# Optimization experiments

Measured on AMD Instinct MI355X. Metric: run time of the kernel, lower is better.

## Reference

```python
import jax, jax.numpy as jnp
import numpy as np
from jax import lax

OC, IC, K = 256, 256, 3
PAD, STRIDE = 1, 1
NNZ = 59000
N, H, W = 32, 56, 56


def setup_inputs() -> dict:
    key = jax.random.key(0)
    k1, k2, k3, k4 = jax.random.split(key, 4)
    x = jax.random.normal(k1, (N, IC, H, W), dtype=jnp.float32)
    W_val = jax.random.normal(k2, (NNZ,), dtype=jnp.float32)
    W_idx = jax.random.randint(k3, (NNZ,), 0, OC * IC * K * K, dtype=jnp.int64)
    bias = jax.random.normal(k4, (OC,), dtype=jnp.float32)
    return {"x": x, "W_val": W_val, "W_idx": W_idx, "bias": bias}


def reference(x, W_val, W_idx, bias):
    # Scatter COO values into the dense [OC, IC, K, K] weight (duplicates sum).
    dense_w = jnp.zeros((OC * IC * K * K,), dtype=W_val.dtype).at[W_idx].add(W_val)
    dense_w = dense_w.reshape(OC, IC, K, K)
    # conv2d, NCHW / OIHW layout, stride=STRIDE, symmetric padding=PAD
    out = lax.conv_general_dilated(
        x, dense_w,
        window_strides=(STRIDE, STRIDE),
        padding=[(PAD, PAD), (PAD, PAD)],
        dimension_numbers=("NCHW", "OIHW", "NCHW"),
    )
    out = out + bias[None, :, None, None]
    return out
```

## Files before the change

kernel.cpp:

```cpp
#include <hip/hip_runtime.h>

typedef unsigned short ushort;
typedef __attribute__((ext_vector_type(8))) short bf16x8;
typedef __attribute__((ext_vector_type(4))) float f32x4;
typedef __attribute__((ext_vector_type(4))) ushort us4;

#define NBATCH 32
#define ICN 256
#define OCN 256
#define HSZ 56
#define WSZ 56
#define HP 58
#define SPAT (HP*HP)
#define KTOT 2304
#define MTOT (NBATCH*HSZ*WSZ)
#define NT   (KTOT/64)

#define XP_BYTES ((size_t)NBATCH*SPAT*ICN*2)
#define WD_BYTES ((size_t)OCN*KTOT*4)

__device__ __forceinline__ ushort f2bf(float f) {
  union { float f; unsigned u; } c; c.f = f;
  unsigned r = c.u + 0x7FFFu + ((c.u >> 16) & 1u);
  return (ushort)(r >> 16);
}

__global__ void k_transpose(const float* __restrict__ x, ushort* __restrict__ xp) {
  __shared__ float tile[ICN*57];
  int h = blockIdx.x, n = blockIdx.y;
  ushort* dst = xp + ((size_t)n*SPAT + (size_t)h*HP)*ICN;
  if (h == 0 || h == HP-1) {
    for (int e = threadIdx.x; e < HP*ICN/4; e += 256) ((us4*)dst)[e] = (us4){0,0,0,0};
    return;
  }
  const float* src = x + ((size_t)n*ICN*HSZ*WSZ) + (size_t)(h-1)*WSZ;
  for (int e = threadIdx.x; e < ICN*WSZ; e += 256) {
    int ic = e / WSZ, w = e - ic*WSZ;
    tile[ic*57 + w] = src[(size_t)ic*(HSZ*WSZ) + w];
  }
  __syncthreads();
  for (int e = threadIdx.x; e < ICN*HP; e += 256) {
    int w = e >> 8, ic = e & 255;
    dst[e] = (w == 0 || w == HP-1) ? (ushort)0 : f2bf(tile[ic*57 + (w-1)]);
  }
}

__global__ void k_scatter(const int* __restrict__ idx, const float* __restrict__ val,
                          float* __restrict__ wd, int nnz) {
  int i = blockIdx.x*256 + threadIdx.x;
  if (i >= nnz) return;
  int id = idx[i];
  int oc = id / (ICN*9);
  int rem = id - oc*(ICN*9);
  int ic = rem / 9;
  int k9 = rem - ic*9;
  atomicAdd(wd + (size_t)oc*KTOT + k9*ICN + ic, val[i]);
}

__global__ void k_convert3(const float* __restrict__ wd, ushort* __restrict__ bm3) {
  int e = blockIdx.x*256 + threadIdx.x;
  int lam = e & 63;
  int f   = (e >> 6) & 3;
  int wc  = (e >> 8) & 3;
  int kh  = (e >> 10) & 1;
  int t   = e >> 11;
  int oc  = wc*64 + f*16 + (lam & 15);
  int k   = (t >> 2)*256 + (t & 3)*64 + kh*32 + (lam >> 4)*8;
  const float* src = wd + (size_t)oc*KTOT + k;
  float4 v0 = *(const float4*)(src);
  float4 v1 = *(const float4*)(src + 4);
  us4 lo, hi;
  lo[0]=f2bf(v0.x); lo[1]=f2bf(v0.y); lo[2]=f2bf(v0.z); lo[3]=f2bf(v0.w);
  hi[0]=f2bf(v1.x); hi[1]=f2bf(v1.y); hi[2]=f2bf(v1.z); hi[3]=f2bf(v1.w);
  ushort* dst = bm3 + (size_t)e*8;
  *(us4*)(dst) = lo; *(us4*)(dst+4) = hi;
}


#define GLD(gsrc, ldst) __builtin_amdgcn_global_load_lds( \
    (const __attribute__((address_space(1))) void*)(gsrc), \
    (__attribute__((address_space(3))) void*)(ldst), 16, 0, 0)
#define BAR()  asm volatile("s_barrier" ::: "memory")
#define VMW(N) do { asm volatile("s_waitcnt vmcnt(" #N ")" ::: "memory"); \
                    __builtin_amdgcn_sched_barrier(0); } while (0)
#define LGKM(N) do { asm volatile("s_waitcnt lgkmcnt(" #N ")" ::: "memory"); \
                     __builtin_amdgcn_sched_barrier(0); } while (0)

#define STAGE_AU(T1, U) do { \
    const int t4_ = (T1) >> 2; const int khh_ = t4_/3, khw_ = t4_ - khh_*3; \
    const int koff_ = (khh_*HP + khw_)*256 + (((T1) & 3) << 6); \
    ushort* d_ = &Ab[(((T1)&1)*16384) + (U)*8192]; \
    GLD(xp + ((U) ? srcA10 : srcA00) + koff_, d_ + ldsOff0); \
    GLD(xp + ((U) ? srcA11 : srcA01) + koff_, d_ + ldsOff1); } while (0)

#define GLB(DST, VOFF) \
    asm volatile("global_load_dwordx4 %0, %4, %5 offset:0\n\t" \
                 "global_load_dwordx4 %1, %4, %5 offset:1024\n\t" \
                 "global_load_dwordx4 %2, %4, %5 offset:2048\n\t" \
                 "global_load_dwordx4 %3, %4, %5 offset:3072" \
                 : "=&v"(DST[0]), "=&v"(DST[1]), "=&v"(DST[2]), "=&v"(DST[3]) \
                 : "v"(VOFF), "s"(bm3) : "memory")

#define LOADA_TO(DST, KH, MH, C) do { \
    unsigned a_ = ((KH) ? aL1v : aL0v) + (unsigned)((C)*32768 + (MH)*8192); \
    asm volatile("ds_read_b128 %0, %4 offset:0\n\t" \
                 "ds_read_b128 %1, %4 offset:2048\n\t" \
                 "ds_read_b128 %2, %4 offset:4096\n\t" \
                 "ds_read_b128 %3, %4 offset:6144" \
                 : "=&v"(DST[0]), "=&v"(DST[1]), "=&v"(DST[2]), "=&v"(DST[3]) \
                 : "v"(a_)); } while (0)

#define MFMA16(MH, AV, BV) do { \
    __builtin_amdgcn_s_setprio(1); \
    _Pragma("unroll") \
    for (int f_ = 0; f_ < 4; ++f_) { \
      _Pragma("unroll") \
      for (int n_ = 0; n_ < 4; ++n_) \
        acc[(MH)*4+f_][n_] = __builtin_amdgcn_mfma_f32_16x16x32_bf16( \
            AV[f_], BV[n_], acc[(MH)*4+f_][n_], 0, 0, 0); \
    } \
    __builtin_amdgcn_s_setprio(0); } while (0)

__global__ __launch_bounds__(512, 2) void k_gemm8(const ushort* __restrict__ xp,
                                                  const ushort* __restrict__ bm3,
                                                  const float* __restrict__ bias,
                                                  float* __restrict__ out) {
  __shared__ __align__(128) ushort Ab[2*2*128*64];

  const int tid = threadIdx.x;
  const int lam = tid & 63;
  const int wv  = tid >> 6;
  const int wr  = wv >> 2;
  const int wc  = wv & 3;
  const int la  = lam & 15;
  const int m0  = blockIdx.x * 256;

  const unsigned AbB = (unsigned)(uintptr_t)(__attribute__((address_space(3))) char*)Ab;

  const int q0 = (lam >> 4) ^ (la & 7);
  const unsigned aL0v = AbB + wr*16384 + la*128 + q0*16;
  const unsigned aL1v = AbB + wr*16384 + la*128 + (q0 ^ 4)*16;

  const unsigned wcB = wc*4096 + lam*16;

  const int ldsOff0 = (0*8 + wv)*512;
  const int ldsOff1 = (1*8 + wv)*512;
  int srcA00, srcA01, srcA10, srcA11;
  {
    const int oA = (lam & 7) ^ (lam >> 3);
    int m, n, rem, oh, ow, r;
    r = (0*8 + wv)*8 + (lam >> 3);
    m = m0 + 0*128 + r; n = m/3136; rem = m - n*3136; oh = rem/56; ow = rem - oh*56;
    srcA00 = (n*SPAT + oh*HP + ow)*ICN + oA*8;
    r = (1*8 + wv)*8 + (lam >> 3);
    m = m0 + 0*128 + r; n = m/3136; rem = m - n*3136; oh = rem/56; ow = rem - oh*56;
    srcA01 = (n*SPAT + oh*HP + ow)*ICN + oA*8;
    r = (0*8 + wv)*8 + (lam >> 3);
    m = m0 + 1*128 + r; n = m/3136; rem = m - n*3136; oh = rem/56; ow = rem - oh*56;
    srcA10 = (n*SPAT + oh*HP + ow)*ICN + oA*8;
    r = (1*8 + wv)*8 + (lam >> 3);
    m = m0 + 1*128 + r; n = m/3136; rem = m - n*3136; oh = rem/56; ow = rem - oh*56;
    srcA11 = (n*SPAT + oh*HP + ow)*ICN + oA*8;
  }

  f32x4 acc[8][4];
#pragma unroll
  for (int a = 0; a < 8; ++a)
#pragma unroll
    for (int b = 0; b < 4; ++b) acc[a][b] = (f32x4){0.f, 0.f, 0.f, 0.f};

  bf16x8 av00_[4], av01_[4], av10_[4], av11_[4], bvA_[4], bvB_[4];

  STAGE_AU(0, 0); STAGE_AU(0, 1);
  GLB(bvA_, wcB);
  VMW(4);
  BAR();

  for (int t = 0; t < NT-1; ++t) {
    const int c = t & 1;
    const unsigned vb = (unsigned)t*32768 + wcB;
    LOADA_TO(av00_, 0, 0, c); LOADA_TO(av01_, 0, 1, c);
    LOADA_TO(av10_, 1, 0, c); LOADA_TO(av11_, 1, 1, c);
    GLB(bvB_, vb + 16384);
    STAGE_AU(t+1, 0);
    VMW(6);
    LGKM(12);
    MFMA16(0, av00_, bvA_);
    STAGE_AU(t+1, 1);
    LGKM(8);
    MFMA16(1, av01_, bvA_);
    GLB(bvA_, vb + 32768);
    VMW(8);
    LGKM(4);
    MFMA16(0, av10_, bvB_);
    LGKM(0);
    MFMA16(1, av11_, bvB_);
    VMW(4);
    BAR();
  }

  {
    const int c = (NT-1) & 1;
    const unsigned vb = (unsigned)(NT-1)*32768 + wcB;
    LOADA_TO(av00_, 0, 0, c); LOADA_TO(av01_, 0, 1, c);
    LOADA_TO(av10_, 1, 0, c); LOADA_TO(av11_, 1, 1, c);
    GLB(bvB_, vb + 16384);
    VMW(4);
    LGKM(12);
    MFMA16(0, av00_, bvA_);
    LGKM(8);
    MFMA16(1, av01_, bvA_);
    VMW(0);
    LGKM(4);
    MFMA16(0, av10_, bvB_);
    LGKM(0);
    MFMA16(1, av11_, bvB_);
  }

#pragma unroll
  for (int nn = 0; nn < 4; ++nn) {
    int oc = wc*64 + nn*16 + la;
    float bvs = bias[oc];
#pragma unroll
    for (int mf = 0; mf < 8; ++mf) {
      int m = m0 + wr*128 + mf*16 + ((lam >> 4) << 2);
      int n = m / 3136;
      int rem = m - n*3136;
      float4 o;
      o.x = acc[mf][nn][0] + bvs;
      o.y = acc[mf][nn][1] + bvs;
      o.z = acc[mf][nn][2] + bvs;
      o.w = acc[mf][nn][3] + bvs;
      *(float4*)(out + ((size_t)(n*OCN + oc))*3136 + rem) = o;
    }
  }
}

extern "C" void kernel_launch(void* const* d_in, const int* in_sizes, int n_in,
                              void* d_out, int out_size, void* d_ws, size_t ws_size,
                              hipStream_t stream) {
  const float* x    = (const float*)d_in[0];
  const float* wval = (const float*)d_in[1];
  const int*   widx = (const int*)d_in[2];
  const float* bias = (const float*)d_in[3];
  float* out = (float*)d_out;
  const int nnz = in_sizes[1];

  char* ws = (char*)d_ws;
  ushort* xp  = (ushort*)ws;
  float*  wd  = (float*)(ws + XP_BYTES);
  ushort* bm3 = (ushort*)(ws + XP_BYTES + WD_BYTES);

  hipMemsetAsync(wd, 0, WD_BYTES, stream);
  k_transpose<<<dim3(HP, NBATCH), 256, 0, stream>>>(x, xp);
  k_scatter<<<dim3((nnz + 255)/256), 256, 0, stream>>>(widx, wval, wd, nnz);
  k_convert3<<<dim3((NT*2*16*64)/256), 256, 0, stream>>>(wd, bm3);
  k_gemm8<<<dim3(MTOT/256), 512, 0, stream>>>(xp, bm3, bias, out);
}
```

Measured before the change: 183.1 us.

## Triple-buffer A tiles in GEMM and convert to bf16 before transpose

The implicit-GEMM conv kernel moves from a double-buffered to a triple-buffered LDS ring for the A (input patch) tiles. Tiles are prefetched two steps ahead, and LDS fragment reads are interleaved with the MFMA groups in a software pipeline that now uses two barriers per iteration. Separately, the transpose kernel converts to bf16 while staging into shared memory and writes 4-element vectors, which shrinks the LDS tile and the store count. The ring costs 96KB of LDS per block, which may threaten two blocks per CU, and it needs more careful wait-count sequencing.

```diff
diff --git a/kernel.cpp b/kernel.cpp
--- a/kernel.cpp
+++ b/kernel.cpp
@@ -26,7 +26,7 @@
 }
 
 __global__ void k_transpose(const float* __restrict__ x, ushort* __restrict__ xp) {
-  __shared__ float tile[ICN*57];
+  __shared__ ushort t2[WSZ*264];
   int h = blockIdx.x, n = blockIdx.y;
   ushort* dst = xp + ((size_t)n*SPAT + (size_t)h*HP)*ICN;
   if (h == 0 || h == HP-1) {
@@ -36,12 +36,14 @@
   const float* src = x + ((size_t)n*ICN*HSZ*WSZ) + (size_t)(h-1)*WSZ;
   for (int e = threadIdx.x; e < ICN*WSZ; e += 256) {
     int ic = e / WSZ, w = e - ic*WSZ;
-    tile[ic*57 + w] = src[(size_t)ic*(HSZ*WSZ) + w];
+    t2[w*264 + ic] = f2bf(src[(size_t)ic*(HSZ*WSZ) + w]);
   }
   __syncthreads();
-  for (int e = threadIdx.x; e < ICN*HP; e += 256) {
-    int w = e >> 8, ic = e & 255;
-    dst[e] = (w == 0 || w == HP-1) ? (ushort)0 : f2bf(tile[ic*57 + (w-1)]);
+  for (int e4 = threadIdx.x; e4 < HP*ICN/4; e4 += 256) {
+    int wp = e4 >> 6, ic4 = (e4 & 63) << 2;
+    us4 v = (wp == 0 || wp == HP-1) ? (us4){0,0,0,0}
+                                    : *(const us4*)&t2[(wp-1)*264 + ic4];
+    ((us4*)dst)[e4] = v;
   }
 }
 
@@ -86,10 +88,10 @@
 #define LGKM(N) do { asm volatile("s_waitcnt lgkmcnt(" #N ")" ::: "memory"); \
                      __builtin_amdgcn_sched_barrier(0); } while (0)
 
-#define STAGE_AU(T1, U) do { \
+#define STAGE_AU(T1, U, BF) do { \
     const int t4_ = (T1) >> 2; const int khh_ = t4_/3, khw_ = t4_ - khh_*3; \
     const int koff_ = (khh_*HP + khw_)*256 + (((T1) & 3) << 6); \
-    ushort* d_ = &Ab[(((T1)&1)*16384) + (U)*8192]; \
+    ushort* d_ = &Ab[(BF)*16384 + (U)*8192]; \
     GLD(xp + ((U) ? srcA10 : srcA00) + koff_, d_ + ldsOff0); \
     GLD(xp + ((U) ? srcA11 : srcA01) + koff_, d_ + ldsOff1); } while (0)
 
@@ -101,8 +103,8 @@
                  : "=&v"(DST[0]), "=&v"(DST[1]), "=&v"(DST[2]), "=&v"(DST[3]) \
                  : "v"(VOFF), "s"(bm3) : "memory")
 
-#define LOADA_TO(DST, KH, MH, C) do { \
-    unsigned a_ = ((KH) ? aL1v : aL0v) + (unsigned)((C)*32768 + (MH)*8192); \
+#define LOADA_TO(DST, KH, MH, BFB) do { \
+    unsigned a_ = ((KH) ? aL1v : aL0v) + (unsigned)((BFB) + (MH)*8192); \
     asm volatile("ds_read_b128 %0, %4 offset:0\n\t" \
                  "ds_read_b128 %1, %4 offset:2048\n\t" \
                  "ds_read_b128 %2, %4 offset:4096\n\t" \
@@ -125,7 +127,7 @@
                                                   const ushort* __restrict__ bm3,
                                                   const float* __restrict__ bias,
                                                   float* __restrict__ out) {
-  __shared__ __align__(128) ushort Ab[2*2*128*64];
+  __shared__ __align__(128) ushort Ab[3*16384];
 
   const int tid = threadIdx.x;
   const int lam = tid & 63;
@@ -169,52 +171,84 @@
 #pragma unroll
     for (int b = 0; b < 4; ++b) acc[a][b] = (f32x4){0.f, 0.f, 0.f, 0.f};
 
-  bf16x8 av00_[4], av01_[4], av10_[4], av11_[4], bvA_[4], bvB_[4];
-
-  STAGE_AU(0, 0); STAGE_AU(0, 1);
+  bf16x8 avq0_[4], avq1_[4], avq2_[4], avq3_[4], bvA_[4], bvB_[4];
+
+  STAGE_AU(0, 0, 0); STAGE_AU(0, 1, 0);
+  STAGE_AU(1, 0, 1); STAGE_AU(1, 1, 1);
   GLB(bvA_, wcB);
   VMW(4);
   BAR();
-
-  for (int t = 0; t < NT-1; ++t) {
-    const int c = t & 1;
+  LOADA_TO(avq0_, 0, 0, 0); LOADA_TO(avq1_, 0, 1, 0);
+
+  int bf0 = 0, bf1 = 1, bf2 = 2;
+  for (int t = 0; t < NT-2; ++t) {
+    const int b0b = bf0*32768, b1b = bf1*32768;
     const unsigned vb = (unsigned)t*32768 + wcB;
-    LOADA_TO(av00_, 0, 0, c); LOADA_TO(av01_, 0, 1, c);
-    LOADA_TO(av10_, 1, 0, c); LOADA_TO(av11_, 1, 1, c);
+    LOADA_TO(avq2_, 1, 0, b0b);
     GLB(bvB_, vb + 16384);
-    STAGE_AU(t+1, 0);
-    VMW(6);
-    LGKM(12);
-    MFMA16(0, av00_, bvA_);
-    STAGE_AU(t+1, 1);
-    LGKM(8);
-    MFMA16(1, av01_, bvA_);
+    VMW(4);
+    LGKM(8);
+    MFMA16(0, avq0_, bvA_);
+    LOADA_TO(avq3_, 1, 1, b0b);
+    STAGE_AU(t+2, 0, bf2);
+    LGKM(8);
+    MFMA16(1, avq1_, bvA_);
+    BAR();
+    LOADA_TO(avq0_, 0, 0, b1b);
+    STAGE_AU(t+2, 1, bf2);
+    VMW(4);
+    LGKM(8);
+    MFMA16(0, avq2_, bvB_);
+    LOADA_TO(avq1_, 0, 1, b1b);
     GLB(bvA_, vb + 32768);
-    VMW(8);
-    LGKM(4);
-    MFMA16(0, av10_, bvB_);
-    LGKM(0);
-    MFMA16(1, av11_, bvB_);
-    VMW(4);
-    BAR();
+    LGKM(8);
+    MFMA16(1, avq3_, bvB_);
+    BAR();
+    int bt = bf0; bf0 = bf1; bf1 = bf2; bf2 = bt;
   }
 
   {
-    const int c = (NT-1) & 1;
-    const unsigned vb = (unsigned)(NT-1)*32768 + wcB;
-    LOADA_TO(av00_, 0, 0, c); LOADA_TO(av01_, 0, 1, c);
-    LOADA_TO(av10_, 1, 0, c); LOADA_TO(av11_, 1, 1, c);
+    const int t = NT-2;
+    const int b0b = bf0*32768, b1b = bf1*32768;
+    const unsigned vb = (unsigned)t*32768 + wcB;
+    LOADA_TO(avq2_, 1, 0, b0b);
     GLB(bvB_, vb + 16384);
     VMW(4);
-    LGKM(12);
-    MFMA16(0, av00_, bvA_);
-    LGKM(8);
-    MFMA16(1, av01_, bvA_);
+    LGKM(8);
+    MFMA16(0, avq0_, bvA_);
+    LOADA_TO(avq3_, 1, 1, b0b);
+    LGKM(8);
+    MFMA16(1, avq1_, bvA_);
+    BAR();
+    LOADA_TO(avq0_, 0, 0, b1b);
+    VMW(0);
+    LGKM(8);
+    MFMA16(0, avq2_, bvB_);
+    LOADA_TO(avq1_, 0, 1, b1b);
+    GLB(bvA_, vb + 32768);
+    LGKM(8);
+    MFMA16(1, avq3_, bvB_);
+    BAR();
+    int bt = bf0; bf0 = bf1; bf1 = bf2; bf2 = bt;
+  }
+
+  {
+    const int t = NT-1;
+    const int b0b = bf0*32768;
+    const unsigned vb = (unsigned)t*32768 + wcB;
+    LOADA_TO(avq2_, 1, 0, b0b);
+    GLB(bvB_, vb + 16384);
+    VMW(4);
+    LGKM(8);
+    MFMA16(0, avq0_, bvA_);
+    LOADA_TO(avq3_, 1, 1, b0b);
+    LGKM(8);
+    MFMA16(1, avq1_, bvA_);
     VMW(0);
     LGKM(4);
-    MFMA16(0, av10_, bvB_);
+    MFMA16(0, avq2_, bvB_);
     LGKM(0);
-    MFMA16(1, av11_, bvB_);
+    MFMA16(1, avq3_, bvB_);
   }
 
 #pragma unroll
```

Result: faster. 160.3 us (-12.5%).

## Triple-buffer A tiles with 224-row blocks and vectorized bf16 transpose

Applied to the files above, without the earlier changes.

The GEMM M-tile shrinks from 256 to 224 rows, giving 448 blocks instead of 392, which likely spreads better across CUs. The smaller tile frees enough LDS for a three-stage A ring buffer, so staging runs two K-steps ahead, and LDS reads are split into 4+3 fragment groups interleaved with MFMAs. The transpose kernel now converts to bf16 before storing to shared memory and writes 4-element vectors. The trade-offs are more complex pipeline bookkeeping, an idle eighth wave during staging, and lower per-block reuse of B.

```diff
diff --git a/kernel.cpp b/kernel.cpp
--- a/kernel.cpp
+++ b/kernel.cpp
@@ -15,6 +15,7 @@
 #define KTOT 2304
 #define MTOT (NBATCH*HSZ*WSZ)
 #define NT   (KTOT/64)
+#define BM   224
 
 #define XP_BYTES ((size_t)NBATCH*SPAT*ICN*2)
 #define WD_BYTES ((size_t)OCN*KTOT*4)
@@ -26,7 +27,7 @@
 }
 
 __global__ void k_transpose(const float* __restrict__ x, ushort* __restrict__ xp) {
-  __shared__ float tile[ICN*57];
+  __shared__ ushort t2[WSZ*264];
   int h = blockIdx.x, n = blockIdx.y;
   ushort* dst = xp + ((size_t)n*SPAT + (size_t)h*HP)*ICN;
   if (h == 0 || h == HP-1) {
@@ -36,12 +37,14 @@
   const float* src = x + ((size_t)n*ICN*HSZ*WSZ) + (size_t)(h-1)*WSZ;
   for (int e = threadIdx.x; e < ICN*WSZ; e += 256) {
     int ic = e / WSZ, w = e - ic*WSZ;
-    tile[ic*57 + w] = src[(size_t)ic*(HSZ*WSZ) + w];
+    t2[w*264 + ic] = f2bf(src[(size_t)ic*(HSZ*WSZ) + w]);
   }
   __syncthreads();
-  for (int e = threadIdx.x; e < ICN*HP; e += 256) {
-    int w = e >> 8, ic = e & 255;
-    dst[e] = (w == 0 || w == HP-1) ? (ushort)0 : f2bf(tile[ic*57 + (w-1)]);
+  for (int e4 = threadIdx.x; e4 < HP*ICN/4; e4 += 256) {
+    int wp = e4 >> 6, ic4 = (e4 & 63) << 2;
+    us4 v = (wp == 0 || wp == HP-1) ? (us4){0,0,0,0}
+                                    : *(const us4*)&t2[(wp-1)*264 + ic4];
+    ((us4*)dst)[e4] = v;
   }
 }
 
@@ -86,12 +89,15 @@
 #define LGKM(N) do { asm volatile("s_waitcnt lgkmcnt(" #N ")" ::: "memory"); \
                      __builtin_amdgcn_sched_barrier(0); } while (0)
 
-#define STAGE_AU(T1, U) do { \
-    const int t4_ = (T1) >> 2; const int khh_ = t4_/3, khw_ = t4_ - khh_*3; \
-    const int koff_ = (khh_*HP + khw_)*256 + (((T1) & 3) << 6); \
-    ushort* d_ = &Ab[(((T1)&1)*16384) + (U)*8192]; \
-    GLD(xp + ((U) ? srcA10 : srcA00) + koff_, d_ + ldsOff0); \
-    GLD(xp + ((U) ? srcA11 : srcA01) + koff_, d_ + ldsOff1); } while (0)
+#define BUF_US  14848
+#define BUF_B   29696
+
+#define STAGE2X(T2, PAIR, BUFUS) do { \
+    const int t4_ = (T2) >> 2; const int khh_ = t4_/3, khw_ = t4_ - khh_*3; \
+    const int koff_ = (khh_*HP + khw_)*256 + (((T2) & 3) << 6); \
+    ushort* b_ = Ab + (BUFUS); \
+    GLD(xp + ((PAIR) ? sA2 : sA0) + koff_, b_ + ((PAIR) ? dO2 : dO0)); \
+    GLD(xp + ((PAIR) ? sA3 : sA1) + koff_, b_ + ((PAIR) ? dO3 : dO1)); } while (0)
 
 #define GLB(DST, VOFF) \
     asm volatile("global_load_dwordx4 %0, %4, %5 offset:0\n\t" \
@@ -101,8 +107,8 @@
                  : "=&v"(DST[0]), "=&v"(DST[1]), "=&v"(DST[2]), "=&v"(DST[3]) \
                  : "v"(VOFF), "s"(bm3) : "memory")
 
-#define LOADA_TO(DST, KH, MH, C) do { \
-    unsigned a_ = ((KH) ? aL1v : aL0v) + (unsigned)((C)*32768 + (MH)*8192); \
+#define LOADA4(DST, KH, BFB) do { \
+    unsigned a_ = ((KH) ? aL1v : aL0v) + (unsigned)(BFB); \
     asm volatile("ds_read_b128 %0, %4 offset:0\n\t" \
                  "ds_read_b128 %1, %4 offset:2048\n\t" \
                  "ds_read_b128 %2, %4 offset:4096\n\t" \
@@ -110,14 +116,33 @@
                  : "=&v"(DST[0]), "=&v"(DST[1]), "=&v"(DST[2]), "=&v"(DST[3]) \
                  : "v"(a_)); } while (0)
 
-#define MFMA16(MH, AV, BV) do { \
+#define LOADA3(DST, KH, BFB) do { \
+    unsigned a_ = ((KH) ? aL1v : aL0v) + (unsigned)((BFB) + 8192); \
+    asm volatile("ds_read_b128 %0, %3 offset:0\n\t" \
+                 "ds_read_b128 %1, %3 offset:2048\n\t" \
+                 "ds_read_b128 %2, %3 offset:4096" \
+                 : "=&v"(DST[0]), "=&v"(DST[1]), "=&v"(DST[2]) \
+                 : "v"(a_)); } while (0)
+
+#define MFMA16(AV, BV) do { \
     __builtin_amdgcn_s_setprio(1); \
     _Pragma("unroll") \
     for (int f_ = 0; f_ < 4; ++f_) { \
       _Pragma("unroll") \
       for (int n_ = 0; n_ < 4; ++n_) \
-        acc[(MH)*4+f_][n_] = __builtin_amdgcn_mfma_f32_16x16x32_bf16( \
-            AV[f_], BV[n_], acc[(MH)*4+f_][n_], 0, 0, 0); \
+        acc[f_][n_] = __builtin_amdgcn_mfma_f32_16x16x32_bf16( \
+            AV[f_], BV[n_], acc[f_][n_], 0, 0, 0); \
+    } \
+    __builtin_amdgcn_s_setprio(0); } while (0)
+
+#define MFMA12(AV, BV) do { \
+    __builtin_amdgcn_s_setprio(1); \
+    _Pragma("unroll") \
+    for (int f_ = 0; f_ < 3; ++f_) { \
+      _Pragma("unroll") \
+      for (int n_ = 0; n_ < 4; ++n_) \
+        acc[4+f_][n_] = __builtin_amdgcn_mfma_f32_16x16x32_bf16( \
+            AV[f_], BV[n_], acc[4+f_][n_], 0, 0, 0); \
     } \
     __builtin_amdgcn_s_setprio(0); } while (0)
 
@@ -125,7 +150,7 @@
                                                   const ushort* __restrict__ bm3,
                                                   const float* __restrict__ bias,
                                                   float* __restrict__ out) {
-  __shared__ __align__(128) ushort Ab[2*2*128*64];
+  __shared__ __align__(128) ushort Ab[3*BUF_US];
 
   const int tid = threadIdx.x;
   const int lam = tid & 63;
@@ -133,88 +158,119 @@
   const int wr  = wv >> 2;
   const int wc  = wv & 3;
   const int la  = lam & 15;
-  const int m0  = blockIdx.x * 256;
+  const int m0  = blockIdx.x * BM;
 
   const unsigned AbB = (unsigned)(uintptr_t)(__attribute__((address_space(3))) char*)Ab;
 
   const int q0 = (lam >> 4) ^ (la & 7);
-  const unsigned aL0v = AbB + wr*16384 + la*128 + q0*16;
-  const unsigned aL1v = AbB + wr*16384 + la*128 + (q0 ^ 4)*16;
+  const unsigned aL0v = AbB + wr*14336 + la*128 + q0*16;
+  const unsigned aL1v = AbB + wr*14336 + la*128 + (q0 ^ 4)*16;
 
   const unsigned wcB = wc*4096 + lam*16;
 
-  const int ldsOff0 = (0*8 + wv)*512;
-  const int ldsOff1 = (1*8 + wv)*512;
-  int srcA00, srcA01, srcA10, srcA11;
-  {
+  int sA0, sA1, sA2, sA3;
+  int dO0, dO1, dO2, dO3;
+  if (wv < 7) {
     const int oA = (lam & 7) ^ (lam >> 3);
     int m, n, rem, oh, ow, r;
-    r = (0*8 + wv)*8 + (lam >> 3);
-    m = m0 + 0*128 + r; n = m/3136; rem = m - n*3136; oh = rem/56; ow = rem - oh*56;
-    srcA00 = (n*SPAT + oh*HP + ow)*ICN + oA*8;
-    r = (1*8 + wv)*8 + (lam >> 3);
-    m = m0 + 0*128 + r; n = m/3136; rem = m - n*3136; oh = rem/56; ow = rem - oh*56;
-    srcA01 = (n*SPAT + oh*HP + ow)*ICN + oA*8;
-    r = (0*8 + wv)*8 + (lam >> 3);
-    m = m0 + 1*128 + r; n = m/3136; rem = m - n*3136; oh = rem/56; ow = rem - oh*56;
-    srcA10 = (n*SPAT + oh*HP + ow)*ICN + oA*8;
-    r = (1*8 + wv)*8 + (lam >> 3);
-    m = m0 + 1*128 + r; n = m/3136; rem = m - n*3136; oh = rem/56; ow = rem - oh*56;
-    srcA11 = (n*SPAT + oh*HP + ow)*ICN + oA*8;
-  }
-
-  f32x4 acc[8][4];
+    r = (wv*4 + 0)*8 + (lam >> 3);
+    m = m0 + r; n = m/3136; rem = m - n*3136; oh = rem/56; ow = rem - oh*56;
+    sA0 = (n*SPAT + oh*HP + ow)*ICN + oA*8;  dO0 = (wv*4 + 0)*512;
+    r = (wv*4 + 1)*8 + (lam >> 3);
+    m = m0 + r; n = m/3136; rem = m - n*3136; oh = rem/56; ow = rem - oh*56;
+    sA1 = (n*SPAT + oh*HP + ow)*ICN + oA*8;  dO1 = (wv*4 + 1)*512;
+    r = (wv*4 + 2)*8 + (lam >> 3);
+    m = m0 + r; n = m/3136; rem = m - n*3136; oh = rem/56; ow = rem - oh*56;
+    sA2 = (n*SPAT + oh*HP + ow)*ICN + oA*8;  dO2 = (wv*4 + 2)*512;
+    r = (wv*4 + 3)*8 + (lam >> 3);
+    m = m0 + r; n = m/3136; rem = m - n*3136; oh = rem/56; ow = rem - oh*56;
+    sA3 = (n*SPAT + oh*HP + ow)*ICN + oA*8;  dO3 = (wv*4 + 3)*512;
+  } else {
+    sA0 = sA1 = sA2 = sA3 = 0;
+    dO0 = dO1 = dO2 = dO3 = 14336;
+  }
+
+  f32x4 acc[7][4];
 #pragma unroll
-  for (int a = 0; a < 8; ++a)
+  for (int a = 0; a < 7; ++a)
 #pragma unroll
     for (int b = 0; b < 4; ++b) acc[a][b] = (f32x4){0.f, 0.f, 0.f, 0.f};
 
-  bf16x8 av00_[4], av01_[4], av10_[4], av11_[4], bvA_[4], bvB_[4];
-
-  STAGE_AU(0, 0); STAGE_AU(0, 1);
+  bf16x8 avq0_[4], avq1_[3], avq2_[4], avq3_[3], bvA_[4], bvB_[4];
+
+  STAGE2X(0, 0, 0);       STAGE2X(0, 1, 0);
+  STAGE2X(1, 0, BUF_US);  STAGE2X(1, 1, BUF_US);
   GLB(bvA_, wcB);
   VMW(4);
   BAR();
-
-  for (int t = 0; t < NT-1; ++t) {
-    const int c = t & 1;
+  LOADA4(avq0_, 0, 0); LOADA3(avq1_, 0, 0);
+
+  int bf0b = 0, bf1b = BUF_B, bf2b = 2*BUF_B;
+  int bf2u = 2*BUF_US;
+  for (int t = 0; t < NT-2; ++t) {
     const unsigned vb = (unsigned)t*32768 + wcB;
-    LOADA_TO(av00_, 0, 0, c); LOADA_TO(av01_, 0, 1, c);
-    LOADA_TO(av10_, 1, 0, c); LOADA_TO(av11_, 1, 1, c);
-    GLB(bvB_, vb + 16384);
-    STAGE_AU(t+1, 0);
-    VMW(6);
-    LGKM(12);
-    MFMA16(0, av00_, bvA_);
-    STAGE_AU(t+1, 1);
-    LGKM(8);
-    MFMA16(1, av01_, bvA_);
-    GLB(bvA_, vb + 32768);
-    VMW(8);
-    LGKM(4);
-    MFMA16(0, av10_, bvB_);
-    LGKM(0);
-    MFMA16(1, av11_, bvB_);
-    VMW(4);
-    BAR();
-  }
-
-  {
-    const int c = (NT-1) & 1;
-    const unsigned vb = (unsigned)(NT-1)*32768 + wcB;
-    LOADA_TO(av00_, 0, 0, c); LOADA_TO(av01_, 0, 1, c);
-    LOADA_TO(av10_, 1, 0, c); LOADA_TO(av11_, 1, 1, c);
+    LOADA4(avq2_, 1, bf0b);
     GLB(bvB_, vb + 16384);
     VMW(4);
-    LGKM(12);
-    MFMA16(0, av00_, bvA_);
-    LGKM(8);
-    MFMA16(1, av01_, bvA_);
+    LGKM(7);
+    MFMA16(avq0_, bvA_);
+    LOADA3(avq3_, 1, bf0b);
+    STAGE2X(t+2, 0, bf2u);
+    LGKM(7);
+    MFMA12(avq1_, bvA_);
+    BAR();
+    LOADA4(avq0_, 0, bf1b);
+    STAGE2X(t+2, 1, bf2u);
+    VMW(4);
+    LGKM(7);
+    MFMA16(avq2_, bvB_);
+    LOADA3(avq1_, 0, bf1b);
+    GLB(bvA_, vb + 32768);
+    LGKM(7);
+    MFMA12(avq3_, bvB_);
+    BAR();
+    int bt = bf0b; bf0b = bf1b; bf1b = bf2b; bf2b = bt;
+    bf2u = bf2b / 2;
+  }
+
+  {
+    const unsigned vb = (unsigned)(NT-2)*32768 + wcB;
+    LOADA4(avq2_, 1, bf0b);
+    GLB(bvB_, vb + 16384);
+    VMW(4);
+    LGKM(7);
+    MFMA16(avq0_, bvA_);
+    LOADA3(avq3_, 1, bf0b);
+    LGKM(7);
+    MFMA12(avq1_, bvA_);
+    BAR();
+    LOADA4(avq0_, 0, bf1b);
     VMW(0);
-    LGKM(4);
-    MFMA16(0, av10_, bvB_);
+    LGKM(7);
+    MFMA16(avq2_, bvB_);
+    LOADA3(avq1_, 0, bf1b);
+    GLB(bvA_, vb + 32768);
+    LGKM(7);
+    MFMA12(avq3_, bvB_);
+    BAR();
+    int bt = bf0b; bf0b = bf1b; bf1b = bf2b; bf2b = bt;
+  }
+
+  {
+    const unsigned vb = (unsigned)(NT-1)*32768 + wcB;
+    LOADA4(avq2_, 1, bf0b);
+    GLB(bvB_, vb + 16384);
+    VMW(4);
+    LGKM(7);
+    MFMA16(avq0_, bvA_);
+    LOADA3(avq3_, 1, bf0b);
+    LGKM(7);
+    MFMA12(avq1_, bvA_);
+    VMW(0);
+    LGKM(3);
+    MFMA16(avq2_, bvB_);
     LGKM(0);
-    MFMA16(1, av11_, bvB_);
+    MFMA12(avq3_, bvB_);
   }
 
 #pragma unroll
@@ -222,8 +278,8 @@
     int oc = wc*64 + nn*16 + la;
     float bvs = bias[oc];
 #pragma unroll
-    for (int mf = 0; mf < 8; ++mf) {
-      int m = m0 + wr*128 + mf*16 + ((lam >> 4) << 2);
+    for (int mf = 0; mf < 7; ++mf) {
+      int m = m0 + wr*112 + mf*16 + ((lam >> 4) << 2);
       int n = m / 3136;
       int rem = m - n*3136;
       float4 o;
@@ -255,5 +311,5 @@
   k_transpose<<<dim3(HP, NBATCH), 256, 0, stream>>>(x, xp);
   k_scatter<<<dim3((nnz + 255)/256), 256, 0, stream>>>(widx, wval, wd, nnz);
   k_convert3<<<dim3((NT*2*16*64)/256), 256, 0, stream>>>(wd, bm3);
-  k_gemm8<<<dim3(MTOT/256), 512, 0, stream>>>(xp, bm3, bias, out);
-}
+  k_gemm8<<<dim3(MTOT/BM), 512, 0, stream>>>(xp, bm3, bias, out);
+}
```

Result: faster. 149.4 us, median of 2 (-18.4%).
